# Kernel optimization log

Hardware: AMD Instinct MI355X
Metric: run time of the kernel (lower is better)

Reference implementation:

```python
import jax, jax.numpy as jnp
import numpy as np

H = 16          # num_heads
LN_EPS = 1e-5   # torch LayerNorm default


def _ln(x, g, b):
    m = jnp.mean(x, axis=-1, keepdims=True)
    v = jnp.var(x, axis=-1, keepdims=True)
    return (x - m) * jax.lax.rsqrt(v + LN_EPS) * g + b


def _cross_attn(xq, xkv, wq, wk, wv, wp, bp):
    B, N, C = xq.shape
    d = C // H
    scale = d ** -0.5
    q = (xq @ wq).reshape(B, N, H, d).transpose(0, 2, 1, 3)   # bhnd
    k = (xkv @ wk).reshape(B, N, H, d).transpose(0, 2, 1, 3)
    v = (xkv @ wv).reshape(B, N, H, d).transpose(0, 2, 1, 3)
    attn = jax.nn.softmax(jnp.einsum('bhnd,bhmd->bhnm', q, k) * scale, axis=-1)
    out = jnp.einsum('bhnm,bhmd->bhnd', attn, v).transpose(0, 2, 1, 3).reshape(B, N, C)
    return out @ wp + bp


def setup_inputs() -> dict:
    key = jax.random.key(0)
    ks = jax.random.split(key, 16)
    B, N, C, Hid = 8, 1024, 1024, 4096
    s = 0.02
    inp = {
        'x_1': jax.random.normal(ks[0], (B, N, C), jnp.float32),
        'x_2': jax.random.normal(ks[1], (B, N, C), jnp.float32),
        'x_3': jax.random.normal(ks[2], (B, N, C), jnp.float32),
        'ln11_g': jnp.ones((C,), jnp.float32), 'ln11_b': jnp.zeros((C,), jnp.float32),
        'ln12_g': jnp.ones((C,), jnp.float32), 'ln12_b': jnp.zeros((C,), jnp.float32),
        'ln21_g': jnp.ones((C,), jnp.float32), 'ln21_b': jnp.zeros((C,), jnp.float32),
        'ln23_g': jnp.ones((C,), jnp.float32), 'ln23_b': jnp.zeros((C,), jnp.float32),
        'ln2_g': jnp.ones((C,), jnp.float32), 'ln2_b': jnp.zeros((C,), jnp.float32),
        'a1_wq': s * jax.random.normal(ks[3], (C, C), jnp.float32),
        'a1_wk': s * jax.random.normal(ks[4], (C, C), jnp.float32),
        'a1_wv': s * jax.random.normal(ks[5], (C, C), jnp.float32),
        'a1_wp': s * jax.random.normal(ks[6], (C, C), jnp.float32),
        'a1_bp': jnp.zeros((C,), jnp.float32),
        'a2_wq': s * jax.random.normal(ks[7], (C, C), jnp.float32),
        'a2_wk': s * jax.random.normal(ks[8], (C, C), jnp.float32),
        'a2_wv': s * jax.random.normal(ks[9], (C, C), jnp.float32),
        'a2_wp': s * jax.random.normal(ks[10], (C, C), jnp.float32),
        'a2_bp': jnp.zeros((C,), jnp.float32),
        'fc1_w': s * jax.random.normal(ks[11], (C, Hid), jnp.float32),
        'fc1_b': jnp.zeros((Hid,), jnp.float32),
        'fc2_w': s * jax.random.normal(ks[12], (Hid, C), jnp.float32),
        'fc2_b': jnp.zeros((C,), jnp.float32),
    }
    return inp


def reference(x_1, x_2, x_3,
              ln11_g, ln11_b, ln12_g, ln12_b, ln21_g, ln21_b, ln23_g, ln23_b,
              ln2_g, ln2_b,
              a1_wq, a1_wk, a1_wv, a1_wp, a1_bp,
              a2_wq, a2_wk, a2_wv, a2_wp, a2_bp,
              fc1_w, fc1_b, fc2_w, fc2_b):
    # dual cross-attention branches + residual (drop_path/dropout are identity at p=0)
    br1 = _cross_attn(_ln(x_1, ln11_g, ln11_b), _ln(x_2, ln12_g, ln12_b),
                      a1_wq, a1_wk, a1_wv, a1_wp, a1_bp)
    br2 = _cross_attn(_ln(x_1, ln21_g, ln21_b), _ln(x_3, ln23_g, ln23_b),
                      a2_wq, a2_wk, a2_wv, a2_wp, a2_bp)
    x = x_1 + br1 + br2
    # MLP block
    h = jax.nn.gelu(_ln(x, ln2_g, ln2_b) @ fc1_w + fc1_b, approximate=False)
    x = x + (h @ fc2_w + fc2_b)
    return x
```

## Files before the change

kernel.cpp:

```cpp
#include <hip/hip_runtime.h>
#include <hip/hip_bf16.h>
#include <cstdint>

typedef unsigned short u16;
typedef __bf16 v8bf __attribute__((ext_vector_type(8)));
typedef short v4s __attribute__((ext_vector_type(4)));
typedef float v4f __attribute__((ext_vector_type(4)));

__device__ __forceinline__ u16 f2bf(float f) {
  union { float f; uint32_t u; } v; v.f = f;
  return (u16)((v.u + 0x7fffu + ((v.u >> 16) & 1u)) >> 16);
}
__device__ __forceinline__ float bf2f(u16 u) {
  union { uint32_t u; float f; } v; v.u = ((uint32_t)u) << 16; return v.f;
}
__device__ __forceinline__ float ex2(float x) {
  float r; asm("v_exp_f32 %0, %1" : "=v"(r) : "v"(x)); return r;
}

#define GLL16(gsrc, ldst) \
  __builtin_amdgcn_global_load_lds((__attribute__((address_space(1))) void*)(gsrc), \
      (__attribute__((address_space(3))) void*)(ldst), 16, 0, 0)

#define TILE_MAP(blk, bm, bn) \
  int bm = ((blk) & 7) * 8 + (((blk) >> 3) & 7); \
  int bn = (blk) >> 6;

__device__ __forceinline__ void gemm_core(
    const u16* __restrict__ A, const u16* __restrict__ Bt, int K,
    char* la, char* lb, int bm, int bn, int tid, v4f acc[4][4])
{
  int wv = tid >> 6, lane = tid & 63, quad = lane >> 4, lc = lane & 15;
  int wm = wv & 1, wn = wv >> 1;
  for (int kt = 0; kt < K; kt += 64) {
    __syncthreads();
    #pragma unroll
    for (int c0 = 0; c0 < 4; ++c0) {
      int chunk = wv*4 + c0;
      int off = chunk*1024 + lane*16;
      int row = off >> 7;
      int sc  = (off >> 4) & 7;
      int lg  = sc ^ (row & 7);
      GLL16(A  + (size_t)(bm*128 + row) * K + kt + lg*8, la + chunk*1024);
      GLL16(Bt + (size_t)(bn*128 + row) * K + kt + lg*8, lb + chunk*1024);
    }
    __syncthreads();
    #pragma unroll
    for (int kc = 0; kc < 2; ++kc) {
      v8bf af[4], bfr[4];
      #pragma unroll
      for (int r = 0; r < 4; ++r) {
        int row = wm*64 + r*16 + lc;
        int sc = (kc*4 + quad) ^ (row & 7);
        af[r] = *(const v8bf*)(la + row*128 + sc*16);
      }
      #pragma unroll
      for (int c = 0; c < 4; ++c) {
        int row = wn*64 + c*16 + lc;
        int sc = (kc*4 + quad) ^ (row & 7);
        bfr[c] = *(const v8bf*)(lb + row*128 + sc*16);
      }
      #pragma unroll
      for (int r = 0; r < 4; ++r)
        #pragma unroll
        for (int c = 0; c < 4; ++c)
          acc[r][c] = __builtin_amdgcn_mfma_f32_16x16x32_bf16(af[r], bfr[c], acc[r][c], 0, 0, 0);
    }
  }
}

__device__ __forceinline__ void lds_put16(char* lds_, int row, int col, u16 v) {
  *(u16*)(lds_ + row*256 + (((col >> 4) ^ (row & 7)) << 5) + (col & 15)*2) = v;
}
__device__ __forceinline__ void sweep128(const char* lds_, u16* gout, size_t ldc, int tid) {
  int sub = tid >> 4, j = tid & 15;
  #pragma unroll
  for (int p = 0; p < 8; ++p) {
    int row = p*16 + sub;
    uint4 d = *(const uint4*)(lds_ + row*256 + ((((j >> 1) ^ (row & 7)) << 5) + ((j & 1) << 4)));
    *(uint4*)(gout + (size_t)row*ldc + j*8) = d;
  }
}

struct TDesc { const float* W; u16* WT; int K, N, tstart; };

__device__ __forceinline__ void do_transpose(const TDesc& D, int loc, int tid, float* sh) {
  const float* W = D.W;
  u16* WT = D.WT;
  int K = D.K, N = D.N;
  int tiles_n = N >> 5;
  int bn = loc % tiles_n, bk = loc / tiles_n;
  int tx = tid & 31, ty = tid >> 5;
  #pragma unroll
  for (int j = 0; j < 4; ++j)
    sh[(ty + j*8)*33 + tx] = W[(size_t)(bk*32 + ty + j*8) * N + bn*32 + tx];
  __syncthreads();
  #pragma unroll
  for (int j = 0; j < 4; ++j)
    WT[(size_t)(bn*32 + ty + j*8) * K + bk*32 + tx] = f2bf(sh[tx*33 + ty + j*8]);
}

__device__ __forceinline__ void ln_f32_row(const float* x, const float* g, const float* b,
                                           u16* out, int row, int tid, float* red)
{
  float4 v = ((const float4*)(x + (size_t)row * 1024))[tid];
  float s = v.x + v.y + v.z + v.w;
  float ss = v.x*v.x + v.y*v.y + v.z*v.z + v.w*v.w;
  for (int d = 1; d < 64; d <<= 1) { s += __shfl_xor(s, d); ss += __shfl_xor(ss, d); }
  int wv = tid >> 6, lane = tid & 63;
  if (lane == 0) { red[wv] = s; red[4 + wv] = ss; }
  __syncthreads();
  s  = red[0] + red[1] + red[2] + red[3];
  ss = red[4] + red[5] + red[6] + red[7];
  float mean = s * (1.f/1024.f);
  float var  = ss * (1.f/1024.f) - mean*mean;
  float rs = rsqrtf(var + 1e-5f);
  float4 gv = ((const float4*)g)[tid];
  float4 bv = ((const float4*)b)[tid];
  ushort4 o;
  o.x = f2bf((v.x-mean)*rs*gv.x + bv.x);
  o.y = f2bf((v.y-mean)*rs*gv.y + bv.y);
  o.z = f2bf((v.z-mean)*rs*gv.z + bv.z);
  o.w = f2bf((v.w-mean)*rs*gv.w + bv.w);
  ((ushort4*)out)[(size_t)row*256 + tid] = o;
}

__device__ __forceinline__ void ln_f32_row2(const float* x,
    const float* g1, const float* b1, const float* g2, const float* b2,
    u16* o1, u16* o2, int row, int tid, float* red)
{
  float4 v = ((const float4*)(x + (size_t)row * 1024))[tid];
  float s = v.x + v.y + v.z + v.w;
  float ss = v.x*v.x + v.y*v.y + v.z*v.z + v.w*v.w;
  for (int d = 1; d < 64; d <<= 1) { s += __shfl_xor(s, d); ss += __shfl_xor(ss, d); }
  int wv = tid >> 6, lane = tid & 63;
  if (lane == 0) { red[wv] = s; red[4 + wv] = ss; }
  __syncthreads();
  s  = red[0] + red[1] + red[2] + red[3];
  ss = red[4] + red[5] + red[6] + red[7];
  float mean = s * (1.f/1024.f);
  float var  = ss * (1.f/1024.f) - mean*mean;
  float rs = rsqrtf(var + 1e-5f);
  float4 xn;
  xn.x = (v.x-mean)*rs; xn.y = (v.y-mean)*rs; xn.z = (v.z-mean)*rs; xn.w = (v.w-mean)*rs;
  {
    float4 gv = ((const float4*)g1)[tid];
    float4 bv = ((const float4*)b1)[tid];
    ushort4 o;
    o.x = f2bf(xn.x*gv.x + bv.x); o.y = f2bf(xn.y*gv.y + bv.y);
    o.z = f2bf(xn.z*gv.z + bv.z); o.w = f2bf(xn.w*gv.w + bv.w);
    ((ushort4*)o1)[(size_t)row*256 + tid] = o;
  }
  {
    float4 gv = ((const float4*)g2)[tid];
    float4 bv = ((const float4*)b2)[tid];
    ushort4 o;
    o.x = f2bf(xn.x*gv.x + bv.x); o.y = f2bf(xn.y*gv.y + bv.y);
    o.z = f2bf(xn.z*gv.z + bv.z); o.w = f2bf(xn.w*gv.w + bv.w);
    ((ushort4*)o2)[(size_t)row*256 + tid] = o;
  }
}

struct PrepA {
  TDesc d[3];
  const float *x1, *g11, *b11, *g21, *b21;
  const float *x2, *g12, *b12;
  u16 *xq1, *xq2, *xkv1;
  int tsa;
};
__global__ __launch_bounds__(256) void prep_a_kernel(PrepA P)
{
  __shared__ float sh[32*33];
  int tid = threadIdx.x;
  int bi = blockIdx.x;
  if (bi < P.tsa) {
    int idx = 0;
    #pragma unroll
    for (int i = 1; i < 3; ++i) if (bi >= P.d[i].tstart) idx = i;
    do_transpose(P.d[idx], bi - P.d[idx].tstart, tid, sh);
  } else {
    int lid = bi - P.tsa;
    if (lid < 8192)
      ln_f32_row2(P.x1, P.g11, P.b11, P.g21, P.b21, P.xq1, P.xq2, lid, tid, sh);
    else
      ln_f32_row(P.x2, P.g12, P.b12, P.xkv1, lid - 8192, tid, sh);
  }
}

__global__ __launch_bounds__(256) void ln_bf16_kernel(
    const u16* __restrict__ x, const float* __restrict__ g, const float* __restrict__ bt,
    u16* __restrict__ out)
{
  int row = blockIdx.x, tid = threadIdx.x;
  ushort4 xr = ((const ushort4*)x)[(size_t)row*256 + tid];
  float4 v;
  v.x = bf2f(xr.x); v.y = bf2f(xr.y); v.z = bf2f(xr.z); v.w = bf2f(xr.w);
  float s = v.x + v.y + v.z + v.w;
  float ss = v.x*v.x + v.y*v.y + v.z*v.z + v.w*v.w;
  for (int d = 1; d < 64; d <<= 1) { s += __shfl_xor(s, d); ss += __shfl_xor(ss, d); }
  __shared__ float red[8];
  int wv = tid >> 6, lane = tid & 63;
  if (lane == 0) { red[wv] = s; red[4 + wv] = ss; }
  __syncthreads();
  s  = red[0] + red[1] + red[2] + red[3];
  ss = red[4] + red[5] + red[6] + red[7];
  float mean = s * (1.f/1024.f);
  float var  = ss * (1.f/1024.f) - mean*mean;
  float rs = rsqrtf(var + 1e-5f);
  float4 gv = ((const float4*)g)[tid];
  float4 bv = ((const float4*)bt)[tid];
  ushort4 o;
  o.x = f2bf((v.x-mean)*rs*gv.x + bv.x);
  o.y = f2bf((v.y-mean)*rs*gv.y + bv.y);
  o.z = f2bf((v.z-mean)*rs*gv.z + bv.z);
  o.w = f2bf((v.w-mean)*rs*gv.w + bv.w);
  ((ushort4*)out)[(size_t)row*256 + tid] = o;
}

struct QkvArgs { const u16* A[3]; const u16* Bt[3]; u16* C[3]; };

__device__ __forceinline__ void qkv_body(const QkvArgs& P, int blk, int tid, char* lds_)
{
  int sub = blk >> 9;
  int local = blk & 511;
  TILE_MAP(local, bm, bn)
  int wv = tid >> 6, lane = tid & 63, quad = lane >> 4, lc = lane & 15;
  int wm = wv & 1, wn = wv >> 1;
  v4f acc[4][4] = {};
  gemm_core(P.A[sub], P.Bt[sub], 1024, lds_, lds_ + 16384, bm, bn, tid, acc);
  u16* Cout = P.C[sub];
  __syncthreads();
  if (sub == 2) {
    #pragma unroll
    for (int r = 0; r < 4; ++r) {
      int rl = wm*64 + r*16 + quad*4;
      #pragma unroll
      for (int c = 0; c < 4; ++c) {
        int cl = wn*64 + c*16 + lc;
        #pragma unroll
        for (int i = 0; i < 4; ++i)
          lds_put16(lds_, cl, rl + i, f2bf(acc[r][c][i]));
      }
    }
    __syncthreads();
    sweep128(lds_, Cout + (size_t)(bn*128) * 8192 + bm*128, 8192, tid);
  } else {
    #pragma unroll
    for (int r = 0; r < 4; ++r) {
      int lrow = wm*64 + r*16 + quad*4;
      #pragma unroll
      for (int c = 0; c < 4; ++c) {
        int lcol = wn*64 + c*16 + lc;
        #pragma unroll
        for (int i = 0; i < 4; ++i)
          lds_put16(lds_, lrow + i, lcol, f2bf(acc[r][c][i]));
      }
    }
    __syncthreads();
    sweep128(lds_, Cout + (size_t)(bm*128) * 1024 + bn*128, 1024, tid);
  }
}

__global__ __launch_bounds__(256, 3) void gemm_qkv(QkvArgs P)
{
  __shared__ __align__(16) char lds_[32768];
  qkv_body(P, blockIdx.x, threadIdx.x, lds_);
}

struct PrepB {
  TDesc d[7];
  const float *x3, *g23, *b23;
  u16 *xkv2;
  int tsb;
};
__global__ __launch_bounds__(256, 3) void qkv_prep_kernel(QkvArgs P, PrepB Q)
{
  __shared__ __align__(16) char lds_[32768];
  int tid = threadIdx.x;
  if ((int)blockIdx.x < 1536) {
    qkv_body(P, blockIdx.x, tid, lds_);
  } else {
    float* sh = (float*)lds_;
    int bi = blockIdx.x - 1536;
    if (bi < Q.tsb) {
      int idx = 0;
      #pragma unroll
      for (int i = 1; i < 7; ++i) if (bi >= Q.d[i].tstart) idx = i;
      do_transpose(Q.d[idx], bi - Q.d[idx].tstart, tid, sh);
    } else {
      ln_f32_row(Q.x3, Q.g23, Q.b23, Q.xkv2, bi - Q.tsb, tid, sh);
    }
  }
}

__device__ __forceinline__ void attn_body(
    const u16* __restrict__ Q, const u16* __restrict__ K, const u16* __restrict__ VT,
    u16* __restrict__ O, int bid, int tid, char* lds_)
{
  int qt = bid & 15, h = (bid >> 4) & 15, b = bid >> 8;
  int wv = tid >> 6, lane = tid & 63, quad = lane >> 4, lc = lane & 15;
  char* kt_l = lds_;
  char* vt_l = lds_ + 16384;
  const float cl2 = 0.18033688f;

  v8bf qf[2];
  {
    int qrow = qt*64 + wv*16 + lc;
    const u16* qp = Q + ((size_t)(b*1024 + qrow) * 1024 + h*64 + quad*8);
    qf[0] = *(const v8bf*)qp;
    qf[1] = *(const v8bf*)(qp + 32);
  }

  float m_i = -1e30f, l_i = 0.f;
  v4f oacc[4] = {};

  for (int it = 0; it < 8; ++it) {
    int kvb = it * 128;
    __syncthreads();
    #pragma unroll
    for (int c0 = 0; c0 < 4; ++c0) {
      int ch = wv*4 + c0;
      int off = ch*1024 + lane*16;
      {
        int row = off >> 7, sc = (off >> 4) & 7, lg = sc ^ (row & 7);
        GLL16(K + (size_t)(b*1024 + kvb + row) * 1024 + h*64 + lg*8, kt_l + ch*1024);
      }
      {
        int row = off >> 8, sc = (off >> 4) & 15, lg = sc ^ (row & 15);
        GLL16(VT + (size_t)(h*64 + row) * 8192 + b*1024 + kvb + lg*8, vt_l + ch*1024);
      }
    }
    __syncthreads();

    v4f s[8] = {};
    #pragma unroll
    for (int ct = 0; ct < 8; ++ct) {
      int row = ct*16 + lc;
      #pragma unroll
      for (int kc = 0; kc < 2; ++kc) {
        int sc = (kc*4 + quad) ^ (row & 7);
        v8bf kf = *(const v8bf*)(kt_l + row*128 + sc*16);
        s[ct] = __builtin_amdgcn_mfma_f32_16x16x32_bf16(kf, qf[kc], s[ct], 0, 0, 0);
      }
    }

    #pragma unroll
    for (int ct = 0; ct < 8; ++ct)
      #pragma unroll
      for (int i = 0; i < 4; ++i) s[ct][i] *= cl2;
    float mx = m_i;
    #pragma unroll
    for (int ct = 0; ct < 8; ++ct)
      #pragma unroll
      for (int i = 0; i < 4; ++i) mx = fmaxf(mx, s[ct][i]);
    mx = fmaxf(mx, __shfl_xor(mx, 16));
    mx = fmaxf(mx, __shfl_xor(mx, 32));
    float alpha = ex2(m_i - mx);
    float rs = 0.f;
    #pragma unroll
    for (int ct = 0; ct < 8; ++ct)
      #pragma unroll
      for (int i = 0; i < 4; ++i) {
        float p = ex2(s[ct][i] - mx);
        s[ct][i] = p;
        rs += p;
      }
    rs += __shfl_xor(rs, 16);
    rs += __shfl_xor(rs, 32);
    l_i = l_i * alpha + rs;
    m_i = mx;
    #pragma unroll
    for (int dt = 0; dt < 4; ++dt)
      #pragma unroll
      for (int i = 0; i < 4; ++i) oacc[dt][i] *= alpha;

    #pragma unroll
    for (int ct = 0; ct < 8; ++ct) {
      v4s pfrag;
      #pragma unroll
      for (int i = 0; i < 4; ++i) pfrag[i] = (short)f2bf(s[ct][i]);
      int lg = ct*2 + (quad >> 1);
      int ho = (quad & 1) * 8;
      #pragma unroll
      for (int dt = 0; dt < 4; ++dt) {
        int rowd = dt*16 + lc;
        int sc = lg ^ (rowd & 15);
        v4s vfrag = *(const v4s*)(vt_l + rowd*256 + sc*16 + ho);
        oacc[dt] = __builtin_amdgcn_mfma_f32_16x16x16bf16_1k(vfrag, pfrag, oacc[dt], 0, 0, 0);
      }
    }
  }

  __syncthreads();
  {
    char* base = kt_l + wv*2048;
    float inv = 1.f / l_i;
    #pragma unroll
    for (int dt = 0; dt < 4; ++dt) {
      ushort4 o;
      o.x = f2bf(oacc[dt][0]*inv); o.y = f2bf(oacc[dt][1]*inv);
      o.z = f2bf(oacc[dt][2]*inv); o.w = f2bf(oacc[dt][3]*inv);
      int lg = dt*2 + (quad >> 1);
      int sc = lg ^ (lc & 7);
      *(ushort4*)(base + lc*128 + sc*16 + (quad & 1)*8) = o;
    }
  }
  __syncthreads();
  {
    char* base = kt_l + wv*2048;
    #pragma unroll
    for (int rep = 0; rep < 2; ++rep) {
      int qr = rep*8 + (lane >> 3);
      int ch = lane & 7;
      int sc = ch ^ (qr & 7);
      uint4 d = *(const uint4*)(base + qr*128 + sc*16);
      *(uint4*)(O + (size_t)(b*1024 + qt*64 + wv*16 + qr) * 1024 + h*64 + ch*8) = d;
    }
  }
}

__global__ __launch_bounds__(256, 4) void attn_kernel(
    const u16* __restrict__ Q, const u16* __restrict__ K, const u16* __restrict__ VT,
    u16* __restrict__ O)
{
  __shared__ __align__(16) char lds_[32768];
  attn_body(Q, K, VT, O, blockIdx.x, threadIdx.x, lds_);
}

__global__ __launch_bounds__(256, 3) void attn_proj_kernel(
    const u16* __restrict__ Q, const u16* __restrict__ K, const u16* __restrict__ VT,
    u16* __restrict__ O,
    const u16* __restrict__ GA, const u16* __restrict__ GBt,
    const float* __restrict__ Gbias, u16* __restrict__ GC)
{
  __shared__ __align__(16) char lds_[32768];
  int tid = threadIdx.x;
  if ((int)blockIdx.x < 2048) {
    attn_body(Q, K, VT, O, blockIdx.x, tid, lds_);
  } else {
    int local = blockIdx.x - 2048;
    TILE_MAP(local, bm, bn)
    int wv = tid >> 6, lane = tid & 63, quad = lane >> 4, lc = lane & 15;
    int wm = wv & 1, wn = wv >> 1;
    v4f acc[4][4] = {};
    gemm_core(GA, GBt, 1024, lds_, lds_ + 16384, bm, bn, tid, acc);
    __syncthreads();
    #pragma unroll
    for (int r = 0; r < 4; ++r) {
      int lrow = wm*64 + r*16 + quad*4;
      #pragma unroll
      for (int c = 0; c < 4; ++c) {
        int lcol = wn*64 + c*16 + lc;
        float bv = Gbias[bn*128 + lcol];
        #pragma unroll
        for (int i = 0; i < 4; ++i)
          lds_put16(lds_, lrow + i, lcol, f2bf(acc[r][c][i] + bv));
      }
    }
    __syncthreads();
    sweep128(lds_, GC + (size_t)(bm*128) * 1024 + bn*128, 1024, tid);
  }
}

__global__ __launch_bounds__(256, 3) void gemm_projadd(
    const u16* __restrict__ A, const u16* __restrict__ Bt,
    const float* __restrict__ bias, const float* __restrict__ x1,
    const u16* __restrict__ o1b, u16* __restrict__ xsum)
{
  TILE_MAP((int)blockIdx.x, bm, bn)
  int tid = threadIdx.x, wv = tid >> 6, lane = tid & 63, quad = lane >> 4, lc = lane & 15;
  int wm = wv & 1, wn = wv >> 1;
  __shared__ __align__(16) char lds_[32768];
  v4f acc[4][4] = {};
  gemm_core(A, Bt, 1024, lds_, lds_ + 16384, bm, bn, tid, acc);
  __syncthreads();
  #pragma unroll
  for (int r = 0; r < 4; ++r) {
    int lrow = wm*64 + r*16 + quad*4;
    int grow = bm*128 + lrow;
    #pragma unroll
    for (int c = 0; c < 4; ++c) {
      int lcol = wn*64 + c*16 + lc;
      int gcol = bn*128 + lcol;
      float bv = bias[gcol];
      #pragma unroll
      for (int i = 0; i < 4; ++i) {
        size_t idx = (size_t)(grow + i) * 1024 + gcol;
        lds_put16(lds_, lrow + i, lcol, f2bf(acc[r][c][i] + bv + x1[idx] + bf2f(o1b[idx])));
      }
    }
  }
  __syncthreads();
  sweep128(lds_, xsum + (size_t)(bm*128) * 1024 + bn*128, 1024, tid);
}

__global__ __launch_bounds__(256, 2) void gemm_fc1(
    const u16* __restrict__ A, const u16* __restrict__ Bt,
    const float* __restrict__ bias, u16* __restrict__ C)
{
  int bm = blockIdx.x >> 5, bn = blockIdx.x & 31;
  int tid = threadIdx.x, wv = tid >> 6, lane = tid & 63, quad = lane >> 4, lc = lane & 15;
  int wm = wv & 1, wn = wv >> 1;
  __shared__ __align__(16) char lds_[32768];
  v4f acc[4][4] = {};
  gemm_core(A, Bt, 1024, lds_, lds_ + 16384, bm, bn, tid, acc);
  __syncthreads();
  #pragma unroll
  for (int r = 0; r < 4; ++r) {
    int lrow = wm*64 + r*16 + quad*4;
    #pragma unroll
    for (int c = 0; c < 4; ++c) {
      int lcol = wn*64 + c*16 + lc;
      float bv = bias[bn*128 + lcol];
      #pragma unroll
      for (int i = 0; i < 4; ++i) {
        float v = acc[r][c][i] + bv;
        float u2 = fminf(2.3023840f * (v + 0.044715f * v * v * v), 115.f);
        float t = ex2(u2);
        lds_put16(lds_, lrow + i, lcol, f2bf(v * t / (t + 1.f)));
      }
    }
  }
  __syncthreads();
  sweep128(lds_, C + (size_t)(bm*128) * 4096 + bn*128, 4096, tid);
}

__global__ __launch_bounds__(256, 3) void gemm_fc2(
    const u16* __restrict__ A, const u16* __restrict__ Bt,
    const float* __restrict__ bias, const u16* __restrict__ r1,
    float* __restrict__ C)
{
  TILE_MAP((int)blockIdx.x, bm, bn)
  int tid = threadIdx.x, wv = tid >> 6, lane = tid & 63, quad = lane >> 4, lc = lane & 15;
  int wm = wv & 1, wn = wv >> 1;
  __shared__ __align__(16) char lds_[32768];
  v4f acc[4][4] = {};
  gemm_core(A, Bt, 4096, lds_, lds_ + 16384, bm, bn, tid, acc);
  #pragma unroll
  for (int r = 0; r < 4; ++r) {
    int grow = bm*128 + wm*64 + r*16 + quad*4;
    #pragma unroll
    for (int c = 0; c < 4; ++c) {
      int gcol = bn*128 + wn*64 + c*16 + lc;
      float bv = bias[gcol];
      #pragma unroll
      for (int i = 0; i < 4; ++i) {
        size_t idx = (size_t)(grow + i) * 1024 + gcol;
        C[idx] = acc[r][c][i] + bv + bf2f(r1[idx]);
      }
    }
  }
}

extern "C" void kernel_launch(void* const* d_in, const int* in_sizes, int n_in,
                              void* d_out, int out_size, void* d_ws, size_t ws_size,
                              hipStream_t stream)
{
  const float* x1    = (const float*)d_in[0];
  const float* x2    = (const float*)d_in[1];
  const float* x3    = (const float*)d_in[2];
  const float* ln11g = (const float*)d_in[3];
  const float* ln11b = (const float*)d_in[4];
  const float* ln12g = (const float*)d_in[5];
  const float* ln12b = (const float*)d_in[6];
  const float* ln21g = (const float*)d_in[7];
  const float* ln21b = (const float*)d_in[8];
  const float* ln23g = (const float*)d_in[9];
  const float* ln23b = (const float*)d_in[10];
  const float* ln2g  = (const float*)d_in[11];
  const float* ln2b  = (const float*)d_in[12];
  const float* a1wq  = (const float*)d_in[13];
  const float* a1wk  = (const float*)d_in[14];
  const float* a1wv  = (const float*)d_in[15];
  const float* a1wp  = (const float*)d_in[16];
  const float* a1bp  = (const float*)d_in[17];
  const float* a2wq  = (const float*)d_in[18];
  const float* a2wk  = (const float*)d_in[19];
  const float* a2wv  = (const float*)d_in[20];
  const float* a2wp  = (const float*)d_in[21];
  const float* a2bp  = (const float*)d_in[22];
  const float* fc1w  = (const float*)d_in[23];
  const float* fc1b  = (const float*)d_in[24];
  const float* fc2w  = (const float*)d_in[25];
  const float* fc2b  = (const float*)d_in[26];

  char* ws = (char*)d_ws;
  const size_t MB = (size_t)1 << 20;
  u16* wtq1 = (u16*)(ws + 0*MB);  u16* wtk1 = (u16*)(ws + 2*MB);
  u16* wtv1 = (u16*)(ws + 4*MB);  u16* wtp1 = (u16*)(ws + 6*MB);
  u16* wtq2 = (u16*)(ws + 8*MB);  u16* wtk2 = (u16*)(ws + 10*MB);
  u16* wtv2 = (u16*)(ws + 12*MB); u16* wtp2 = (u16*)(ws + 14*MB);
  u16* wtf1 = (u16*)(ws + 16*MB); u16* wtf2 = (u16*)(ws + 24*MB);
  u16* xq1  = (u16*)(ws + 32*MB); u16* xkv1 = (u16*)(ws + 48*MB);
  u16* xq2  = (u16*)(ws + 64*MB); u16* xkv2 = (u16*)(ws + 80*MB);
  u16* Qb   = (u16*)(ws + 96*MB); u16* Kb   = (u16*)(ws + 112*MB);
  u16* VTb  = (u16*)(ws + 128*MB);
  u16* O1   = (u16*)(ws + 32*MB);
  u16* O2   = (u16*)(ws + 48*MB);
  u16* o1b  = (u16*)(ws + 64*MB);
  u16* xsum = (u16*)(ws + 112*MB);
  u16* ln2o = (u16*)(ws + 32*MB);
  u16* hbuf = (u16*)(ws + 48*MB);

  dim3 blk(256);

  PrepA pa;
  {
    const float* Ws[3] = {a1wq, a1wk, a1wv};
    u16* WTs[3]        = {wtq1, wtk1, wtv1};
    int ts = 0;
    for (int i = 0; i < 3; ++i) { pa.d[i] = {Ws[i], WTs[i], 1024, 1024, ts}; ts += 1024; }
    pa.tsa = ts;
  }
  pa.x1 = x1; pa.g11 = ln11g; pa.b11 = ln11b; pa.g21 = ln21g; pa.b21 = ln21b;
  pa.x2 = x2; pa.g12 = ln12g; pa.b12 = ln12b;
  pa.xq1 = xq1; pa.xq2 = xq2; pa.xkv1 = xkv1;
  prep_a_kernel<<<pa.tsa + 16384, blk, 0, stream>>>(pa);

  QkvArgs g1;
  g1.A[0]=xq1;  g1.Bt[0]=wtq1; g1.C[0]=Qb;
  g1.A[1]=xkv1; g1.Bt[1]=wtk1; g1.C[1]=Kb;
  g1.A[2]=xkv1; g1.Bt[2]=wtv1; g1.C[2]=VTb;
  PrepB pb;
  {
    const float* Ws[7] = {a1wp, a2wq, a2wk, a2wv, a2wp, fc1w, fc2w};
    u16* WTs[7]        = {wtp1, wtq2, wtk2, wtv2, wtp2, wtf1, wtf2};
    int Kd[7] = {1024,1024,1024,1024,1024,1024,4096};
    int Nd[7] = {1024,1024,1024,1024,1024,4096,1024};
    int ts = 0;
    for (int i = 0; i < 7; ++i) {
      pb.d[i] = {Ws[i], WTs[i], Kd[i], Nd[i], ts};
      ts += (Kd[i]/32) * (Nd[i]/32);
    }
    pb.tsb = ts;
  }
  pb.x3 = x3; pb.g23 = ln23g; pb.b23 = ln23b; pb.xkv2 = xkv2;
  qkv_prep_kernel<<<1536 + pb.tsb + 8192, blk, 0, stream>>>(g1, pb);

  attn_kernel<<<2048, blk, 0, stream>>>(Qb, Kb, VTb, O1);

  QkvArgs g2;
  g2.A[0]=xq2;  g2.Bt[0]=wtq2; g2.C[0]=Qb;
  g2.A[1]=xkv2; g2.Bt[1]=wtk2; g2.C[1]=Kb;
  g2.A[2]=xkv2; g2.Bt[2]=wtv2; g2.C[2]=VTb;
  gemm_qkv<<<1536, blk, 0, stream>>>(g2);

  attn_proj_kernel<<<2048 + 512, blk, 0, stream>>>(Qb, Kb, VTb, O2, O1, wtp1, a1bp, o1b);

  gemm_projadd<<<512, blk, 0, stream>>>(O2, wtp2, a2bp, x1, o1b, xsum);

  ln_bf16_kernel<<<8192, blk, 0, stream>>>(xsum, ln2g, ln2b, ln2o);

  gemm_fc1<<<2048, blk, 0, stream>>>(ln2o, wtf1, fc1b, hbuf);

  gemm_fc2<<<512, blk, 0, stream>>>(hbuf, wtf2, fc2b, xsum, (float*)d_out);
}
```

Baseline: 693.5 us.

## Fuse attention-1 with branch-2 QKV GEMM and consolidate prep into one kernel

```diff
diff --git a/kernel.cpp b/kernel.cpp
--- a/kernel.cpp
+++ b/kernel.cpp
@@ -161,29 +161,32 @@
   }
 }
 
-struct PrepA {
-  TDesc d[3];
+struct PrepAll {
+  TDesc d[10];
   const float *x1, *g11, *b11, *g21, *b21;
   const float *x2, *g12, *b12;
-  u16 *xq1, *xq2, *xkv1;
-  int tsa;
+  const float *x3, *g23, *b23;
+  u16 *xq1, *xq2, *xkv1, *xkv2;
+  int ts;
 };
-__global__ __launch_bounds__(256) void prep_a_kernel(PrepA P)
+__global__ __launch_bounds__(256) void prep_all_kernel(PrepAll P)
 {
   __shared__ float sh[32*33];
   int tid = threadIdx.x;
   int bi = blockIdx.x;
-  if (bi < P.tsa) {
+  if (bi < P.ts) {
     int idx = 0;
     #pragma unroll
-    for (int i = 1; i < 3; ++i) if (bi >= P.d[i].tstart) idx = i;
+    for (int i = 1; i < 10; ++i) if (bi >= P.d[i].tstart) idx = i;
     do_transpose(P.d[idx], bi - P.d[idx].tstart, tid, sh);
   } else {
-    int lid = bi - P.tsa;
+    int lid = bi - P.ts;
     if (lid < 8192)
       ln_f32_row2(P.x1, P.g11, P.b11, P.g21, P.b21, P.xq1, P.xq2, lid, tid, sh);
+    else if (lid < 16384)
+      ln_f32_row(P.x2, P.g12, P.b12, P.xkv1, lid - 8192, tid, sh);
     else
-      ln_f32_row(P.x2, P.g12, P.b12, P.xkv1, lid - 8192, tid, sh);
+      ln_f32_row(P.x3, P.g23, P.b23, P.xkv2, lid - 16384, tid, sh);
   }
 }
 
@@ -261,36 +264,10 @@
   }
 }
 
-__global__ __launch_bounds__(256, 3) void gemm_qkv(QkvArgs P)
+__global__ __launch_bounds__(256, 4) void gemm_qkv(QkvArgs P)
 {
   __shared__ __align__(16) char lds_[32768];
   qkv_body(P, blockIdx.x, threadIdx.x, lds_);
-}
-
-struct PrepB {
-  TDesc d[7];
-  const float *x3, *g23, *b23;
-  u16 *xkv2;
-  int tsb;
-};
-__global__ __launch_bounds__(256, 3) void qkv_prep_kernel(QkvArgs P, PrepB Q)
-{
-  __shared__ __align__(16) char lds_[32768];
-  int tid = threadIdx.x;
-  if ((int)blockIdx.x < 1536) {
-    qkv_body(P, blockIdx.x, tid, lds_);
-  } else {
-    float* sh = (float*)lds_;
-    int bi = blockIdx.x - 1536;
-    if (bi < Q.tsb) {
-      int idx = 0;
-      #pragma unroll
-      for (int i = 1; i < 7; ++i) if (bi >= Q.d[i].tstart) idx = i;
-      do_transpose(Q.d[idx], bi - Q.d[idx].tstart, tid, sh);
-    } else {
-      ln_f32_row(Q.x3, Q.g23, Q.b23, Q.xkv2, bi - Q.tsb, tid, sh);
-    }
-  }
 }
 
 __device__ __forceinline__ void attn_body(
@@ -427,7 +404,19 @@
   attn_body(Q, K, VT, O, blockIdx.x, threadIdx.x, lds_);
 }
 
-__global__ __launch_bounds__(256, 3) void attn_proj_kernel(
+__global__ __launch_bounds__(256, 4) void attn_qkv_kernel(
+    const u16* __restrict__ Q, const u16* __restrict__ K, const u16* __restrict__ VT,
+    u16* __restrict__ O, QkvArgs G)
+{
+  __shared__ __align__(16) char lds_[32768];
+  int tid = threadIdx.x;
+  if ((int)blockIdx.x < 2048)
+    attn_body(Q, K, VT, O, blockIdx.x, tid, lds_);
+  else
+    qkv_body(G, blockIdx.x - 2048, tid, lds_);
+}
+
+__global__ __launch_bounds__(256, 4) void attn_proj_kernel(
     const u16* __restrict__ Q, const u16* __restrict__ K, const u16* __restrict__ VT,
     u16* __restrict__ O,
     const u16* __restrict__ GA, const u16* __restrict__ GBt,
@@ -462,7 +451,7 @@
   }
 }
 
-__global__ __launch_bounds__(256, 3) void gemm_projadd(
+__global__ __launch_bounds__(256, 4) void gemm_projadd(
     const u16* __restrict__ A, const u16* __restrict__ Bt,
     const float* __restrict__ bias, const float* __restrict__ x1,
     const u16* __restrict__ o1b, u16* __restrict__ xsum)
@@ -596,56 +585,62 @@
   u16* Qb   = (u16*)(ws + 96*MB); u16* Kb   = (u16*)(ws + 112*MB);
   u16* VTb  = (u16*)(ws + 128*MB);
   u16* O1   = (u16*)(ws + 32*MB);
-  u16* O2   = (u16*)(ws + 48*MB);
   u16* o1b  = (u16*)(ws + 64*MB);
   u16* xsum = (u16*)(ws + 112*MB);
   u16* ln2o = (u16*)(ws + 32*MB);
   u16* hbuf = (u16*)(ws + 48*MB);
 
+  bool fused23 = (ws_size >= (size_t)176 * MB);
+  u16 *Q2, *K2, *VT2, *O2;
+  if (fused23) {
+    Q2  = (u16*)(ws + 48*MB);
+    K2  = (u16*)(ws + 144*MB);
+    VT2 = (u16*)(ws + 160*MB);
+    O2  = (u16*)(ws + 96*MB);
+  } else {
+    Q2 = Qb; K2 = Kb; VT2 = VTb;
+    O2  = (u16*)(ws + 48*MB);
+  }
+
   dim3 blk(256);
 
-  PrepA pa;
+  PrepAll pa;
   {
-    const float* Ws[3] = {a1wq, a1wk, a1wv};
-    u16* WTs[3]        = {wtq1, wtk1, wtv1};
+    const float* Ws[10]  = {a1wq, a1wk, a1wv, a1wp, a2wq, a2wk, a2wv, a2wp, fc1w, fc2w};
+    u16* WTs[10]         = {wtq1, wtk1, wtv1, wtp1, wtq2, wtk2, wtv2, wtp2, wtf1, wtf2};
+    int Kd[10] = {1024,1024,1024,1024,1024,1024,1024,1024,1024,4096};
+    int Nd[10] = {1024,1024,1024,1024,1024,1024,1024,1024,4096,1024};
     int ts = 0;
-    for (int i = 0; i < 3; ++i) { pa.d[i] = {Ws[i], WTs[i], 1024, 1024, ts}; ts += 1024; }
-    pa.tsa = ts;
+    for (int i = 0; i < 10; ++i) {
+      pa.d[i] = {Ws[i], WTs[i], Kd[i], Nd[i], ts};
+      ts += (Kd[i]/32) * (Nd[i]/32);
+    }
+    pa.ts = ts;
   }
   pa.x1 = x1; pa.g11 = ln11g; pa.b11 = ln11b; pa.g21 = ln21g; pa.b21 = ln21b;
   pa.x2 = x2; pa.g12 = ln12g; pa.b12 = ln12b;
-  pa.xq1 = xq1; pa.xq2 = xq2; pa.xkv1 = xkv1;
-  prep_a_kernel<<<pa.tsa + 16384, blk, 0, stream>>>(pa);
+  pa.x3 = x3; pa.g23 = ln23g; pa.b23 = ln23b;
+  pa.xq1 = xq1; pa.xq2 = xq2; pa.xkv1 = xkv1; pa.xkv2 = xkv2;
+  prep_all_kernel<<<pa.ts + 24576, blk, 0, stream>>>(pa);
 
   QkvArgs g1;
   g1.A[0]=xq1;  g1.Bt[0]=wtq1; g1.C[0]=Qb;
   g1.A[1]=xkv1; g1.Bt[1]=wtk1; g1.C[1]=Kb;
   g1.A[2]=xkv1; g1.Bt[2]=wtv1; g1.C[2]=VTb;
-  PrepB pb;
-  {
-    const float* Ws[7] = {a1wp, a2wq, a2wk, a2wv, a2wp, fc1w, fc2w};
-    u16* WTs[7]        = {wtp1, wtq2, wtk2, wtv2, wtp2, wtf1, wtf2};
-    int Kd[7] = {1024,1024,1024,1024,1024,1024,4096};
-    int Nd[7] = {1024,1024,1024,1024,1024,4096,1024};
-    int ts = 0;
-    for (int i = 0; i < 7; ++i) {
-      pb.d[i] = {Ws[i], WTs[i], Kd[i], Nd[i], ts};
-      ts += (Kd[i]/32) * (Nd[i]/32);
-    }
-    pb.tsb = ts;
-  }
-  pb.x3 = x3; pb.g23 = ln23g; pb.b23 = ln23b; pb.xkv2 = xkv2;
-  qkv_prep_kernel<<<1536 + pb.tsb + 8192, blk, 0, stream>>>(g1, pb);
-
-  attn_kernel<<<2048, blk, 0, stream>>>(Qb, Kb, VTb, O1);
+  gemm_qkv<<<1536, blk, 0, stream>>>(g1);
 
   QkvArgs g2;
-  g2.A[0]=xq2;  g2.Bt[0]=wtq2; g2.C[0]=Qb;
-  g2.A[1]=xkv2; g2.Bt[1]=wtk2; g2.C[1]=Kb;
-  g2.A[2]=xkv2; g2.Bt[2]=wtv2; g2.C[2]=VTb;
-  gemm_qkv<<<1536, blk, 0, stream>>>(g2);
-
-  attn_proj_kernel<<<2048 + 512, blk, 0, stream>>>(Qb, Kb, VTb, O2, O1, wtp1, a1bp, o1b);
+  g2.A[0]=xq2;  g2.Bt[0]=wtq2; g2.C[0]=Q2;
+  g2.A[1]=xkv2; g2.Bt[1]=wtk2; g2.C[1]=K2;
+  g2.A[2]=xkv2; g2.Bt[2]=wtv2; g2.C[2]=VT2;
+  if (fused23) {
+    attn_qkv_kernel<<<2048 + 1536, blk, 0, stream>>>(Qb, Kb, VTb, O1, g2);
+  } else {
+    attn_kernel<<<2048, blk, 0, stream>>>(Qb, Kb, VTb, O1);
+    gemm_qkv<<<1536, blk, 0, stream>>>(g2);
+  }
+
+  attn_proj_kernel<<<2048 + 512, blk, 0, stream>>>(Q2, K2, VT2, O2, O1, wtp1, a1bp, o1b);
 
   gemm_projadd<<<512, blk, 0, stream>>>(O2, wtp2, a2bp, x1, o1b, xsum);
 
```

New measurement: 693.2 us. About the same (-0.0%).
